# Kernel optimization log

Hardware: AMD Instinct MI355X
Metric: run time of the kernel (lower is better)

Reference implementation:

```python
import jax, jax.numpy as jnp
import numpy as np


def _segsum(x):
    """Stable segment-sum. x: (..., l) -> (..., l, l) lower-triangular sums."""
    l = x.shape[-1]
    cs = jnp.cumsum(x, axis=-1)
    seg = cs[..., :, None] - cs[..., None, :]
    mask = jnp.tril(jnp.ones((l, l), dtype=bool))
    return jnp.where(mask, seg, -jnp.inf)


def setup_inputs() -> dict:
    key = jax.random.key(0)
    kx, ka, kb, kc = jax.random.split(key, 4)
    b, s, h, p, n = 4, 8192, 32, 64, 16
    X = jax.random.normal(kx, (b, s, h, p), dtype=jnp.float32)
    # negative A for realistic decaying SSM dynamics / numerical safety
    A = -jnp.abs(jax.random.normal(ka, (b, s, h), dtype=jnp.float32)) * 0.5
    B = jax.random.normal(kb, (b, s, h, n), dtype=jnp.float32)
    C = jax.random.normal(kc, (b, s, h, n), dtype=jnp.float32)
    return {"X": X, "A": A, "B": B, "C": C, "block_len": 64}


def reference(X, A, B, C, block_len):
    b, s, h, p = X.shape
    n = B.shape[-1]
    c = s // block_len
    l = block_len
    # chunk: (b, c, l, ...)
    Xb = X.reshape(b, c, l, h, p)
    Bb = B.reshape(b, c, l, h, n)
    Cb = C.reshape(b, c, l, h, n)
    Ab = A.reshape(b, c, l, h).transpose(0, 3, 1, 2)  # (b, h, c, l)
    A_cumsum = jnp.cumsum(Ab, axis=-1)                # (b, h, c, l)

    # 1) intra-chunk (diagonal) output
    L = jnp.exp(_segsum(Ab))                          # (b, h, c, l, l)
    Y_diag = jnp.einsum("bclhn,bcshn,bhcls,bcshp->bclhp", Cb, Bb, L, Xb)

    # 2) intra-chunk states (chunk-final state contribution)
    decay_states = jnp.exp(A_cumsum[..., -1:] - A_cumsum)   # (b, h, c, l)
    states = jnp.einsum("bclhn,bhcl,bclhp->bchpn", Bb, decay_states, Xb)

    # 3) inter-chunk recurrence (zero initial states)
    A_last = A_cumsum[..., -1]                        # (b, h, c)
    decay_chunk = jnp.exp(_segsum(jnp.pad(A_last, ((0, 0), (0, 0), (1, 0)))))  # (b,h,c+1,c+1)
    states = jnp.concatenate([jnp.zeros_like(states[:, :1]), states], axis=1)  # (b,c+1,h,p,n)
    new_states = jnp.einsum("bhzc,bchpn->bzhpn", decay_chunk, states)
    states = new_states[:, :-1]                       # states entering each chunk

    # 4) state -> output (off-diagonal)
    state_decay_out = jnp.exp(A_cumsum)               # (b, h, c, l)
    Y_off = jnp.einsum("bclhn,bchpn,bhcl->bclhp", Cb, states, state_decay_out)

    Y = (Y_diag + Y_off).reshape(b, s, h, p)
    return Y
```

## Files before the change

kernel.cpp:

```cpp
#include <hip/hip_runtime.h>

#define BB 4
#define SS 8192
#define HH 32
#define PP 64
#define NN 16
#define LL 64
#define CC 128
#define NCHAIN (BB * HH)
#define NCHT (NCHAIN * CC)

typedef __attribute__((ext_vector_type(8))) short bf16x8;
typedef __attribute__((ext_vector_type(4))) short bf16x4;
typedef __attribute__((ext_vector_type(4))) float f32x4;

__device__ inline short f2bf(float f) {
    unsigned u = __builtin_bit_cast(unsigned, f);
    u = (u + 0x7FFFu + ((u >> 16) & 1u)) >> 16;
    return (short)u;
}

__global__ __launch_bounds__(256) void k1_states(
    const float* __restrict__ X, const float* __restrict__ A,
    const float* __restrict__ B, float* __restrict__ states,
    float* __restrict__ alast_g)
{
    int blk = blockIdx.x;
    int h = blk & (HH - 1);
    int c = (blk >> 5) & (CC - 1);
    int b = blk >> 12;
    int tid = threadIdx.x;
    int w = tid >> 6, l = tid & 63, g = l >> 4, lr = l & 15;
    int chain = b * HH + h;

    __shared__ float Bs[LL][17];

    size_t row0 = (size_t)b * SS + (size_t)c * LL;
    const float* Xp = X + (row0 * HH + h) * PP;
    const float* Bp = B + (row0 * HH + h) * NN;
    const float* Ap = A + row0 * HH + h;

    float av = Ap[(size_t)l * HH];
    int r = tid >> 2, q = tid & 3;
    float4 br = *(const float4*)(Bp + (size_t)r * (HH * NN) + q * 4);
    float xr[16];
#pragma unroll
    for (int kt = 0; kt < 2; ++kt)
#pragma unroll
        for (int e = 0; e < 8; ++e)
            xr[kt * 8 + e] = Xp[(size_t)(kt * 32 + g * 8 + e) * (HH * PP) + 16 * w + lr];

    float x = av;
#pragma unroll
    for (int d = 1; d < 64; d <<= 1) {
        float t = __shfl_up(x, d, 64);
        if (l >= d) x += t;
    }
    float alast = __shfl(x, 63, 64);

    float wlr = __expf(alast - __shfl(x, r & 63, 64));
    Bs[r][q * 4 + 0] = br.x * wlr;
    Bs[r][q * 4 + 1] = br.y * wlr;
    Bs[r][q * 4 + 2] = br.z * wlr;
    Bs[r][q * 4 + 3] = br.w * wlr;
    __syncthreads();

    bf16x8 bt[2], xf[2];
#pragma unroll
    for (int kt = 0; kt < 2; ++kt)
#pragma unroll
        for (int e = 0; e < 8; ++e) {
            int row = kt * 32 + g * 8 + e;
            bt[kt][e] = f2bf(Bs[row][lr]);
            xf[kt][e] = f2bf(xr[kt * 8 + e]);
        }
    f32x4 st = __builtin_amdgcn_mfma_f32_16x16x32_bf16(bt[0], xf[0], (f32x4)0.f, 0, 0, 0);
    st = __builtin_amdgcn_mfma_f32_16x16x32_bf16(bt[1], xf[1], st, 0, 0, 0);

    float4 pv = {st[0], st[1], st[2], st[3]};
    *(float4*)(states + (size_t)(chain * CC + c) * (PP * NN) + (16 * w + lr) * NN + 4 * g) = pv;
    if (tid == 0) alast_g[chain * CC + c] = alast;
}

__global__ __launch_bounds__(256) void k2_scan(
    float* __restrict__ states, const float* __restrict__ alast_g)
{
    int chain = blockIdx.x >> 2;
    int t = ((blockIdx.x & 3) << 8) + threadIdx.x;
    __shared__ float eal[CC];
    if (threadIdx.x < CC)
        eal[threadIdx.x] = __expf(alast_g[chain * CC + threadIdx.x]);
    __syncthreads();

    float* base = states + (size_t)chain * CC * (PP * NN) + t;
    float P = 0.f;
    for (int c0 = 0; c0 < CC; c0 += 8) {
        float s[8], o[8];
#pragma unroll
        for (int u = 0; u < 8; ++u) s[u] = base[(size_t)(c0 + u) * (PP * NN)];
#pragma unroll
        for (int u = 0; u < 8; ++u) { o[u] = P; P = eal[c0 + u] * P + s[u]; }
#pragma unroll
        for (int u = 0; u < 8; ++u) base[(size_t)(c0 + u) * (PP * NN)] = o[u];
    }
}

__global__ __launch_bounds__(256) void k3_y(
    const float* __restrict__ X, const float* __restrict__ A,
    const float* __restrict__ Bm, const float* __restrict__ Cm,
    const float* __restrict__ pin, float* __restrict__ Y)
{
    int blk = blockIdx.x;
    int h = blk & (HH - 1);
    int c = (blk >> 5) & (CC - 1);
    int b = blk >> 12;
    int tid = threadIdx.x;
    int w = tid >> 6, l = tid & 63, g = l >> 4, lr = l & 15;
    int chain = b * HH + h;

    __shared__ short XTF[8 * 64 * 8];
    __shared__ short ScF[8 * 64 * 8];
    __shared__ short BsF[4 * 64 * 8];
    __shared__ short PF[4 * 64 * 8];

    size_t row0 = (size_t)b * SS + (size_t)c * LL;
    const float* Xp = X + (row0 * HH + h) * PP;
    const float* Bp = Bm + (row0 * HH + h) * NN;
    const float* Cp = Cm + (row0 * HH + h) * NN;
    const float* Ap = A + row0 * HH + h;
    float* Yp = Y + (row0 * HH + h) * PP;

    float av = Ap[(size_t)l * HH];
    int r = tid >> 2, q = tid & 3;
    float4 br = *(const float4*)(Bp + (size_t)r * (HH * NN) + q * 4);
    float4 cr0 = {0,0,0,0}, cr1 = {0,0,0,0};
    if (g < 2) {
        const float* crp = Cp + (size_t)(16 * w + lr) * (HH * NN) + g * 8;
        cr0 = *(const float4*)crp;
        cr1 = *(const float4*)(crp + 4);
    }
    float4 pinv = *(const float4*)(pin + (size_t)(chain * CC + c) * (PP * NN) + (16 * w + lr) * NN + 4 * g);
    float xr[16];
#pragma unroll
    for (int si = 0; si < 2; ++si) {
        int k0 = si * 32 + g * 8;
#pragma unroll
        for (int e = 0; e < 8; ++e)
            xr[si * 8 + e] = Xp[(size_t)(k0 + e) * (HH * PP) + 16 * w + lr];
    }

    float x = av;
#pragma unroll
    for (int d = 1; d < 64; d <<= 1) {
        float t = __shfl_up(x, d, 64);
        if (l >= d) x += t;
    }
    float cs_i[4], ei[4];
    int ib = 16 * w + 4 * g;
#pragma unroll
    for (int rr = 0; rr < 4; ++rr) {
        cs_i[rr] = __shfl(x, ib + rr, 64);
        ei[rr] = __expf(cs_i[rr]);
    }

    ((bf16x8*)ScF)[tid] = (bf16x8)0;
    ((bf16x8*)ScF)[tid + 256] = (bf16x8)0;
    if (tid < 128)
        ((bf16x8*)PF)[(tid >> 5) * 64 + 32 + (tid & 31)] = (bf16x8)0;
    {
        int fl = (r & 15) + 16 * (q >> 1);
        int jt = r >> 4;
        bf16x4 bb = { f2bf(br.x), f2bf(br.y), f2bf(br.z), f2bf(br.w) };
        ((bf16x4*)BsF)[(jt * 64 + fl) * 2 + (q & 1)] = bb;
        int zt = tid >> 6, zu = (tid >> 1) & 31, zv = tid & 1;
        ((bf16x4*)BsF)[(zt * 64 + 32 + zu) * 2 + zv] = (bf16x4)0;
    }
    {
        float P4[4] = {pinv.x, pinv.y, pinv.z, pinv.w};
#pragma unroll
        for (int rr = 0; rr < 4; ++rr) {
            int n = 4 * g + rr;
            PF[(w * 64 + (n >> 3) * 16 + lr) * 8 + (n & 7)] = f2bf(P4[rr]);
        }
    }
    bf16x8 caw = (bf16x8)0;
    if (g < 2) {
        caw[0] = f2bf(cr0.x); caw[1] = f2bf(cr0.y);
        caw[2] = f2bf(cr0.z); caw[3] = f2bf(cr0.w);
        caw[4] = f2bf(cr1.x); caw[5] = f2bf(cr1.y);
        caw[6] = f2bf(cr1.z); caw[7] = f2bf(cr1.w);
    }
    __syncthreads();

    f32x4 acc[4];
#pragma unroll
    for (int pt = 0; pt < 4; ++pt) {
        bf16x8 pfv = ((bf16x8*)PF)[pt * 64 + l];
        acc[pt] = __builtin_amdgcn_mfma_f32_16x16x32_bf16(caw, pfv, (f32x4)0.f, 0, 0, 0);
    }
#pragma unroll
    for (int pt = 0; pt < 4; ++pt)
#pragma unroll
        for (int rr = 0; rr < 4; ++rr) acc[pt][rr] *= ei[rr];

    for (int jt = 0; jt <= w; ++jt) {
        bf16x8 bw = ((bf16x8*)BsF)[jt * 64 + l];
        f32x4 sr = __builtin_amdgcn_mfma_f32_16x16x32_bf16(caw, bw, (f32x4)0.f, 0, 0, 0);
        int j = jt * 16 + lr;
        float csj = __shfl(x, j, 64);
        int kt2 = j >> 5;
        int flb = 16 * ((j >> 3) & 3);
#pragma unroll
        for (int rr = 0; rr < 4; ++rr) {
            int i15 = g * 4 + rr;
            int i = 16 * w + i15;
            float v = (j <= i) ? sr[rr] * __expf(cs_i[rr] - csj) : 0.f;
            ScF[((w * 2 + kt2) * 64 + i15 + flb) * 8 + (j & 7)] = f2bf(v);
        }
    }

#pragma unroll
    for (int si = 0; si < 2; ++si) {
        bf16x8 xb;
#pragma unroll
        for (int e = 0; e < 8; ++e) xb[e] = f2bf(xr[si * 8 + e]);
        ((bf16x8*)XTF)[tid + si * 256] = xb;
    }
    __syncthreads();

    int kts = (w >= 2) ? 2 : 1;
    for (int kt = 0; kt < kts; ++kt) {
        bf16x8 af = ((bf16x8*)ScF)[(w * 2 + kt) * 64 + l];
#pragma unroll
        for (int pt = 0; pt < 4; ++pt) {
            bf16x8 xf = ((bf16x8*)XTF)[(kt * 4 + pt) * 64 + l];
            acc[pt] = __builtin_amdgcn_mfma_f32_16x16x32_bf16(af, xf, acc[pt], 0, 0, 0);
        }
    }

#pragma unroll
    for (int pt = 0; pt < 4; ++pt)
#pragma unroll
        for (int rr = 0; rr < 4; ++rr)
            Yp[(size_t)(16 * w + 4 * g + rr) * (HH * PP) + pt * 16 + lr] = acc[pt][rr];
}

extern "C" void kernel_launch(void* const* d_in, const int* in_sizes, int n_in,
                              void* d_out, int out_size, void* d_ws, size_t ws_size,
                              hipStream_t stream)
{
    const float* X = (const float*)d_in[0];
    const float* A = (const float*)d_in[1];
    const float* B = (const float*)d_in[2];
    const float* C = (const float*)d_in[3];
    float* Y = (float*)d_out;

    float* states = (float*)d_ws;
    float* alast  = states + (size_t)NCHT * (PP * NN);

    dim3 blk(256);
    k1_states<<<dim3(NCHT), blk, 0, stream>>>(X, A, B, states, alast);
    k2_scan<<<dim3(NCHAIN * 4), blk, 0, stream>>>(states, alast);
    k3_y<<<dim3(NCHT), blk, 0, stream>>>(X, A, B, C, states, Y);
}
```

Before: 276.3 us.

## Process two chunks per block in state and output kernels to raise loads in flight

k1_states and k3_y now each handle two chunks per block, chunk cp and chunk cp+64 of the same chain, so their grids are halved. All global loads for both chunks (X, A, B, C and incoming states) are issued up front into registers, and the shared-memory staging is reused sequentially for the two chunks. The aim is more memory-level parallelism and less per-block setup in these bandwidth-bound kernels. In exchange, register pressure roughly doubles and the block count falls, which can lower occupancy.

```diff
diff --git a/kernel.cpp b/kernel.cpp
--- a/kernel.cpp
+++ b/kernel.cpp
@@ -20,6 +20,16 @@
     return (short)u;
 }
 
+__device__ inline float wscan(float v, int l) {
+    float x = v;
+#pragma unroll
+    for (int d = 1; d < 64; d <<= 1) {
+        float t = __shfl_up(x, d, 64);
+        if (l >= d) x += t;
+    }
+    return x;
+}
+
 __global__ __launch_bounds__(256) void k1_states(
     const float* __restrict__ X, const float* __restrict__ A,
     const float* __restrict__ B, float* __restrict__ states,
@@ -27,59 +37,69 @@
 {
     int blk = blockIdx.x;
     int h = blk & (HH - 1);
-    int c = (blk >> 5) & (CC - 1);
-    int b = blk >> 12;
+    int cp = (blk >> 5) & 63;
+    int b = blk >> 11;
     int tid = threadIdx.x;
     int w = tid >> 6, l = tid & 63, g = l >> 4, lr = l & 15;
     int chain = b * HH + h;
-
-    __shared__ float Bs[LL][17];
-
-    size_t row0 = (size_t)b * SS + (size_t)c * LL;
-    const float* Xp = X + (row0 * HH + h) * PP;
-    const float* Bp = B + (row0 * HH + h) * NN;
-    const float* Ap = A + row0 * HH + h;
-
-    float av = Ap[(size_t)l * HH];
     int r = tid >> 2, q = tid & 3;
-    float4 br = *(const float4*)(Bp + (size_t)r * (HH * NN) + q * 4);
-    float xr[16];
-#pragma unroll
-    for (int kt = 0; kt < 2; ++kt)
-#pragma unroll
-        for (int e = 0; e < 8; ++e)
-            xr[kt * 8 + e] = Xp[(size_t)(kt * 32 + g * 8 + e) * (HH * PP) + 16 * w + lr];
-
-    float x = av;
-#pragma unroll
-    for (int d = 1; d < 64; d <<= 1) {
-        float t = __shfl_up(x, d, 64);
-        if (l >= d) x += t;
-    }
-    float alast = __shfl(x, 63, 64);
-
-    float wlr = __expf(alast - __shfl(x, r & 63, 64));
-    Bs[r][q * 4 + 0] = br.x * wlr;
-    Bs[r][q * 4 + 1] = br.y * wlr;
-    Bs[r][q * 4 + 2] = br.z * wlr;
-    Bs[r][q * 4 + 3] = br.w * wlr;
-    __syncthreads();
-
-    bf16x8 bt[2], xf[2];
-#pragma unroll
-    for (int kt = 0; kt < 2; ++kt)
-#pragma unroll
-        for (int e = 0; e < 8; ++e) {
-            int row = kt * 32 + g * 8 + e;
-            bt[kt][e] = f2bf(Bs[row][lr]);
-            xf[kt][e] = f2bf(xr[kt * 8 + e]);
-        }
-    f32x4 st = __builtin_amdgcn_mfma_f32_16x16x32_bf16(bt[0], xf[0], (f32x4)0.f, 0, 0, 0);
-    st = __builtin_amdgcn_mfma_f32_16x16x32_bf16(bt[1], xf[1], st, 0, 0, 0);
-
-    float4 pv = {st[0], st[1], st[2], st[3]};
-    *(float4*)(states + (size_t)(chain * CC + c) * (PP * NN) + (16 * w + lr) * NN + 4 * g) = pv;
-    if (tid == 0) alast_g[chain * CC + c] = alast;
+
+    __shared__ float Bs[2][LL][17];
+
+    size_t r0 = (size_t)b * SS + (size_t)cp * LL;
+    size_t r1 = r0 + (size_t)64 * LL;
+    const float* Xp0 = X + (r0 * HH + h) * PP;
+    const float* Xp1 = X + (r1 * HH + h) * PP;
+
+    float av0 = (A + r0 * HH + h)[(size_t)l * HH];
+    float av1 = (A + r1 * HH + h)[(size_t)l * HH];
+    float4 br0 = *(const float4*)(B + (r0 * HH + h) * NN + (size_t)r * (HH * NN) + q * 4);
+    float4 br1 = *(const float4*)(B + (r1 * HH + h) * NN + (size_t)r * (HH * NN) + q * 4);
+    float xr0[16], xr1[16];
+#pragma unroll
+    for (int kt = 0; kt < 2; ++kt)
+#pragma unroll
+        for (int e = 0; e < 8; ++e)
+            xr0[kt * 8 + e] = Xp0[(size_t)(kt * 32 + g * 8 + e) * (HH * PP) + 16 * w + lr];
+#pragma unroll
+    for (int kt = 0; kt < 2; ++kt)
+#pragma unroll
+        for (int e = 0; e < 8; ++e)
+            xr1[kt * 8 + e] = Xp1[(size_t)(kt * 32 + g * 8 + e) * (HH * PP) + 16 * w + lr];
+
+    float x0 = wscan(av0, l), x1 = wscan(av1, l);
+    float alast0 = __shfl(x0, 63, 64), alast1 = __shfl(x1, 63, 64);
+    float w0 = __expf(alast0 - __shfl(x0, r, 64));
+    float w1 = __expf(alast1 - __shfl(x1, r, 64));
+    Bs[0][r][q * 4 + 0] = br0.x * w0;
+    Bs[0][r][q * 4 + 1] = br0.y * w0;
+    Bs[0][r][q * 4 + 2] = br0.z * w0;
+    Bs[0][r][q * 4 + 3] = br0.w * w0;
+    Bs[1][r][q * 4 + 0] = br1.x * w1;
+    Bs[1][r][q * 4 + 1] = br1.y * w1;
+    Bs[1][r][q * 4 + 2] = br1.z * w1;
+    Bs[1][r][q * 4 + 3] = br1.w * w1;
+    __syncthreads();
+
+#define K1_CHUNK(U, xr_, c_) { \
+    bf16x8 bt0, bt1, xf0, xf1; \
+    _Pragma("unroll") for (int e = 0; e < 8; ++e) { \
+        bt0[e] = f2bf(Bs[U][g * 8 + e][lr]); \
+        bt1[e] = f2bf(Bs[U][32 + g * 8 + e][lr]); \
+        xf0[e] = f2bf(xr_[e]); xf1[e] = f2bf(xr_[8 + e]); } \
+    f32x4 st = __builtin_amdgcn_mfma_f32_16x16x32_bf16(bt0, xf0, (f32x4)0.f, 0, 0, 0); \
+    st = __builtin_amdgcn_mfma_f32_16x16x32_bf16(bt1, xf1, st, 0, 0, 0); \
+    float4 pv = {st[0], st[1], st[2], st[3]}; \
+    *(float4*)(states + (size_t)(chain * CC + (c_)) * (PP * NN) + (16 * w + lr) * NN + 4 * g) = pv; }
+
+    K1_CHUNK(0, xr0, cp)
+    K1_CHUNK(1, xr1, cp + 64)
+#undef K1_CHUNK
+
+    if (tid == 0) {
+        alast_g[chain * CC + cp] = alast0;
+        alast_g[chain * CC + cp + 64] = alast1;
+    }
 }
 
 __global__ __launch_bounds__(256) void k2_scan(
@@ -112,137 +132,140 @@
 {
     int blk = blockIdx.x;
     int h = blk & (HH - 1);
-    int c = (blk >> 5) & (CC - 1);
-    int b = blk >> 12;
+    int cp = (blk >> 5) & 63;
+    int b = blk >> 11;
     int tid = threadIdx.x;
     int w = tid >> 6, l = tid & 63, g = l >> 4, lr = l & 15;
     int chain = b * HH + h;
+    int r = tid >> 2, q = tid & 3;
 
     __shared__ short XTF[8 * 64 * 8];
     __shared__ short ScF[8 * 64 * 8];
     __shared__ short BsF[4 * 64 * 8];
     __shared__ short PF[4 * 64 * 8];
 
-    size_t row0 = (size_t)b * SS + (size_t)c * LL;
-    const float* Xp = X + (row0 * HH + h) * PP;
-    const float* Bp = Bm + (row0 * HH + h) * NN;
-    const float* Cp = Cm + (row0 * HH + h) * NN;
-    const float* Ap = A + row0 * HH + h;
-    float* Yp = Y + (row0 * HH + h) * PP;
-
-    float av = Ap[(size_t)l * HH];
-    int r = tid >> 2, q = tid & 3;
-    float4 br = *(const float4*)(Bp + (size_t)r * (HH * NN) + q * 4);
-    float4 cr0 = {0,0,0,0}, cr1 = {0,0,0,0};
+    size_t r0 = (size_t)b * SS + (size_t)cp * LL;
+    size_t r1 = r0 + (size_t)64 * LL;
+    const float* Xp0 = X + (r0 * HH + h) * PP;
+    const float* Xp1 = X + (r1 * HH + h) * PP;
+    float* Yp0 = Y + (r0 * HH + h) * PP;
+    float* Yp1 = Y + (r1 * HH + h) * PP;
+
+    float av0 = (A + r0 * HH + h)[(size_t)l * HH];
+    float av1 = (A + r1 * HH + h)[(size_t)l * HH];
+    float4 br0 = *(const float4*)(Bm + (r0 * HH + h) * NN + (size_t)r * (HH * NN) + q * 4);
+    float4 br1 = *(const float4*)(Bm + (r1 * HH + h) * NN + (size_t)r * (HH * NN) + q * 4);
+    float4 cr00 = {0,0,0,0}, cr10 = {0,0,0,0}, cr01 = {0,0,0,0}, cr11 = {0,0,0,0};
     if (g < 2) {
-        const float* crp = Cp + (size_t)(16 * w + lr) * (HH * NN) + g * 8;
-        cr0 = *(const float4*)crp;
-        cr1 = *(const float4*)(crp + 4);
-    }
-    float4 pinv = *(const float4*)(pin + (size_t)(chain * CC + c) * (PP * NN) + (16 * w + lr) * NN + 4 * g);
-    float xr[16];
-#pragma unroll
-    for (int si = 0; si < 2; ++si) {
-        int k0 = si * 32 + g * 8;
-#pragma unroll
-        for (int e = 0; e < 8; ++e)
-            xr[si * 8 + e] = Xp[(size_t)(k0 + e) * (HH * PP) + 16 * w + lr];
-    }
-
-    float x = av;
-#pragma unroll
-    for (int d = 1; d < 64; d <<= 1) {
-        float t = __shfl_up(x, d, 64);
-        if (l >= d) x += t;
-    }
-    float cs_i[4], ei[4];
-    int ib = 16 * w + 4 * g;
-#pragma unroll
-    for (int rr = 0; rr < 4; ++rr) {
-        cs_i[rr] = __shfl(x, ib + rr, 64);
-        ei[rr] = __expf(cs_i[rr]);
-    }
-
-    ((bf16x8*)ScF)[tid] = (bf16x8)0;
-    ((bf16x8*)ScF)[tid + 256] = (bf16x8)0;
+        const float* cp0 = Cm + (r0 * HH + h) * NN + (size_t)(16 * w + lr) * (HH * NN) + g * 8;
+        const float* cp1 = Cm + (r1 * HH + h) * NN + (size_t)(16 * w + lr) * (HH * NN) + g * 8;
+        cr00 = *(const float4*)cp0; cr10 = *(const float4*)(cp0 + 4);
+        cr01 = *(const float4*)cp1; cr11 = *(const float4*)(cp1 + 4);
+    }
+    int pnoff = (16 * w + lr) * NN + 4 * g;
+    float4 pinv0 = *(const float4*)(pin + (size_t)(chain * CC + cp) * (PP * NN) + pnoff);
+    float4 pinv1 = *(const float4*)(pin + (size_t)(chain * CC + cp + 64) * (PP * NN) + pnoff);
+    float xr0[16], xr1[16];
+#pragma unroll
+    for (int kt = 0; kt < 2; ++kt)
+#pragma unroll
+        for (int e = 0; e < 8; ++e)
+            xr0[kt * 8 + e] = Xp0[(size_t)(kt * 32 + g * 8 + e) * (HH * PP) + 16 * w + lr];
+#pragma unroll
+    for (int kt = 0; kt < 2; ++kt)
+#pragma unroll
+        for (int e = 0; e < 8; ++e)
+            xr1[kt * 8 + e] = Xp1[(size_t)(kt * 32 + g * 8 + e) * (HH * PP) + 16 * w + lr];
+
+    float x0 = wscan(av0, l), x1 = wscan(av1, l);
+
+    ((bf16x8*)ScF)[w * 128 + l] = (bf16x8)0;
+    ((bf16x8*)ScF)[w * 128 + 64 + l] = (bf16x8)0;
     if (tid < 128)
         ((bf16x8*)PF)[(tid >> 5) * 64 + 32 + (tid & 31)] = (bf16x8)0;
     {
-        int fl = (r & 15) + 16 * (q >> 1);
-        int jt = r >> 4;
-        bf16x4 bb = { f2bf(br.x), f2bf(br.y), f2bf(br.z), f2bf(br.w) };
-        ((bf16x4*)BsF)[(jt * 64 + fl) * 2 + (q & 1)] = bb;
         int zt = tid >> 6, zu = (tid >> 1) & 31, zv = tid & 1;
         ((bf16x4*)BsF)[(zt * 64 + 32 + zu) * 2 + zv] = (bf16x4)0;
     }
-    {
-        float P4[4] = {pinv.x, pinv.y, pinv.z, pinv.w};
-#pragma unroll
-        for (int rr = 0; rr < 4; ++rr) {
-            int n = 4 * g + rr;
-            PF[(w * 64 + (n >> 3) * 16 + lr) * 8 + (n & 7)] = f2bf(P4[rr]);
-        }
-    }
-    bf16x8 caw = (bf16x8)0;
-    if (g < 2) {
-        caw[0] = f2bf(cr0.x); caw[1] = f2bf(cr0.y);
-        caw[2] = f2bf(cr0.z); caw[3] = f2bf(cr0.w);
-        caw[4] = f2bf(cr1.x); caw[5] = f2bf(cr1.y);
-        caw[6] = f2bf(cr1.z); caw[7] = f2bf(cr1.w);
-    }
-    __syncthreads();
-
+
+    bf16x8 caw;
     f32x4 acc[4];
-#pragma unroll
-    for (int pt = 0; pt < 4; ++pt) {
-        bf16x8 pfv = ((bf16x8*)PF)[pt * 64 + l];
-        acc[pt] = __builtin_amdgcn_mfma_f32_16x16x32_bf16(caw, pfv, (f32x4)0.f, 0, 0, 0);
-    }
-#pragma unroll
-    for (int pt = 0; pt < 4; ++pt)
-#pragma unroll
-        for (int rr = 0; rr < 4; ++rr) acc[pt][rr] *= ei[rr];
-
-    for (int jt = 0; jt <= w; ++jt) {
-        bf16x8 bw = ((bf16x8*)BsF)[jt * 64 + l];
-        f32x4 sr = __builtin_amdgcn_mfma_f32_16x16x32_bf16(caw, bw, (f32x4)0.f, 0, 0, 0);
-        int j = jt * 16 + lr;
-        float csj = __shfl(x, j, 64);
-        int kt2 = j >> 5;
-        int flb = 16 * ((j >> 3) & 3);
-#pragma unroll
-        for (int rr = 0; rr < 4; ++rr) {
-            int i15 = g * 4 + rr;
-            int i = 16 * w + i15;
-            float v = (j <= i) ? sr[rr] * __expf(cs_i[rr] - csj) : 0.f;
-            ScF[((w * 2 + kt2) * 64 + i15 + flb) * 8 + (j & 7)] = f2bf(v);
-        }
-    }
-
-#pragma unroll
-    for (int si = 0; si < 2; ++si) {
-        bf16x8 xb;
-#pragma unroll
-        for (int e = 0; e < 8; ++e) xb[e] = f2bf(xr[si * 8 + e]);
-        ((bf16x8*)XTF)[tid + si * 256] = xb;
-    }
-    __syncthreads();
-
-    int kts = (w >= 2) ? 2 : 1;
-    for (int kt = 0; kt < kts; ++kt) {
-        bf16x8 af = ((bf16x8*)ScF)[(w * 2 + kt) * 64 + l];
-#pragma unroll
-        for (int pt = 0; pt < 4; ++pt) {
-            bf16x8 xf = ((bf16x8*)XTF)[(kt * 4 + pt) * 64 + l];
-            acc[pt] = __builtin_amdgcn_mfma_f32_16x16x32_bf16(af, xf, acc[pt], 0, 0, 0);
-        }
-    }
-
-#pragma unroll
-    for (int pt = 0; pt < 4; ++pt)
-#pragma unroll
-        for (int rr = 0; rr < 4; ++rr)
-            Yp[(size_t)(16 * w + 4 * g + rr) * (HH * PP) + pt * 16 + lr] = acc[pt][rr];
+    float cs_i[4], ei[4];
+
+#define K3_STAGE(br_, cr0_, cr1_, pinv_) { \
+    int fl = (r & 15) + 16 * (q >> 1); \
+    int jt = r >> 4; \
+    bf16x4 bb = { f2bf(br_.x), f2bf(br_.y), f2bf(br_.z), f2bf(br_.w) }; \
+    ((bf16x4*)BsF)[(jt * 64 + fl) * 2 + (q & 1)] = bb; \
+    bf16x4 pp = { f2bf(pinv_.x), f2bf(pinv_.y), f2bf(pinv_.z), f2bf(pinv_.w) }; \
+    ((bf16x4*)PF)[(w * 64 + (g >> 1) * 16 + lr) * 2 + (g & 1)] = pp; \
+    caw = (bf16x8)0; \
+    if (g < 2) { \
+        caw[0] = f2bf(cr0_.x); caw[1] = f2bf(cr0_.y); caw[2] = f2bf(cr0_.z); caw[3] = f2bf(cr0_.w); \
+        caw[4] = f2bf(cr1_.x); caw[5] = f2bf(cr1_.y); caw[6] = f2bf(cr1_.z); caw[7] = f2bf(cr1_.w); } }
+
+#define K3_PHASE_A(xs_) { \
+    int ib = 16 * w + 4 * g; \
+    _Pragma("unroll") for (int rr = 0; rr < 4; ++rr) { \
+        cs_i[rr] = __shfl(xs_, ib + rr, 64); ei[rr] = __expf(cs_i[rr]); } \
+    _Pragma("unroll") for (int pt = 0; pt < 4; ++pt) { \
+        bf16x8 pfv = ((bf16x8*)PF)[pt * 64 + l]; \
+        acc[pt] = __builtin_amdgcn_mfma_f32_16x16x32_bf16(caw, pfv, (f32x4)0.f, 0, 0, 0); } \
+    _Pragma("unroll") for (int pt = 0; pt < 4; ++pt) \
+        _Pragma("unroll") for (int rr = 0; rr < 4; ++rr) acc[pt][rr] *= ei[rr]; \
+    for (int jt = 0; jt <= w; ++jt) { \
+        bf16x8 bw = ((bf16x8*)BsF)[jt * 64 + l]; \
+        f32x4 sr = __builtin_amdgcn_mfma_f32_16x16x32_bf16(caw, bw, (f32x4)0.f, 0, 0, 0); \
+        int j = jt * 16 + lr; \
+        float csj = __shfl(xs_, j, 64); \
+        int kt2 = j >> 5; \
+        int flb = 16 * ((j >> 3) & 3); \
+        _Pragma("unroll") for (int rr = 0; rr < 4; ++rr) { \
+            int i15 = g * 4 + rr; \
+            int i = 16 * w + i15; \
+            float v = (j <= i) ? sr[rr] * __expf(cs_i[rr] - csj) : 0.f; \
+            ScF[((w * 2 + kt2) * 64 + i15 + flb) * 8 + (j & 7)] = f2bf(v); } } }
+
+#define K3_CONVERT(xr_) { \
+    bf16x8 xb0, xb1; \
+    _Pragma("unroll") for (int e = 0; e < 8; ++e) { xb0[e] = f2bf(xr_[e]); xb1[e] = f2bf(xr_[8 + e]); } \
+    ((bf16x8*)XTF)[tid] = xb0; \
+    ((bf16x8*)XTF)[tid + 256] = xb1; }
+
+#define K3_PHASE_B() { \
+    int kts = (w >= 2) ? 2 : 1; \
+    for (int kt = 0; kt < kts; ++kt) { \
+        bf16x8 af = ((bf16x8*)ScF)[(w * 2 + kt) * 64 + l]; \
+        _Pragma("unroll") for (int pt = 0; pt < 4; ++pt) { \
+            bf16x8 xf = ((bf16x8*)XTF)[(kt * 4 + pt) * 64 + l]; \
+            acc[pt] = __builtin_amdgcn_mfma_f32_16x16x32_bf16(af, xf, acc[pt], 0, 0, 0); } } }
+
+#define K3_STORE(Yp_) { \
+    _Pragma("unroll") for (int pt = 0; pt < 4; ++pt) \
+        _Pragma("unroll") for (int rr = 0; rr < 4; ++rr) \
+            Yp_[(size_t)(16 * w + 4 * g + rr) * (HH * PP) + pt * 16 + lr] = acc[pt][rr]; }
+
+    K3_STAGE(br0, cr00, cr10, pinv0);
+    __syncthreads();
+    K3_PHASE_A(x0);
+    K3_CONVERT(xr0);
+    __syncthreads();
+    K3_PHASE_B();
+    K3_STORE(Yp0);
+
+    K3_STAGE(br1, cr01, cr11, pinv1);
+    __syncthreads();
+    K3_PHASE_A(x1);
+    K3_CONVERT(xr1);
+    __syncthreads();
+    K3_PHASE_B();
+    K3_STORE(Yp1);
+
+#undef K3_STAGE
+#undef K3_PHASE_A
+#undef K3_CONVERT
+#undef K3_PHASE_B
+#undef K3_STORE
 }
 
 extern "C" void kernel_launch(void* const* d_in, const int* in_sizes, int n_in,
@@ -259,7 +282,7 @@
     float* alast  = states + (size_t)NCHT * (PP * NN);
 
     dim3 blk(256);
-    k1_states<<<dim3(NCHT), blk, 0, stream>>>(X, A, B, states, alast);
+    k1_states<<<dim3(NCHT / 2), blk, 0, stream>>>(X, A, B, states, alast);
     k2_scan<<<dim3(NCHAIN * 4), blk, 0, stream>>>(states, alast);
-    k3_y<<<dim3(NCHT), blk, 0, stream>>>(X, A, B, C, states, Y);
-}
+    k3_y<<<dim3(NCHT / 2), blk, 0, stream>>>(X, A, B, C, states, Y);
+}
```

New measurement: 285.9 us. 1.03x slower.

## Store chunk states in bf16 and cache bf16 X fragments for output kernel

Applied to the files above, without the earlier changes.

Chunk states are now written and scanned in bf16 instead of fp32, halving the states traffic in k1, k2 and k3. When the workspace is large enough, k1 also writes the bf16 X fragments in MFMA layout, so k3 reads them contiguously instead of re-reading strided fp32 X. This adds a fresh 128 MB write in k1 and a 128 MB read in k3, in place of k3's 256 MB strided fp32 read. The scan now rounds to bf16 at every step, which may cost accuracy.

```diff
diff --git a/kernel.cpp b/kernel.cpp
--- a/kernel.cpp
+++ b/kernel.cpp
@@ -11,7 +11,7 @@
 #define NCHT (NCHAIN * CC)
 
 typedef __attribute__((ext_vector_type(8))) short bf16x8;
-typedef __attribute__((ext_vector_type(4))) short bf16x4;
+typedef __attribute__((ext_vector_type(4))) short s16x4;
 typedef __attribute__((ext_vector_type(4))) float f32x4;
 
 __device__ inline short f2bf(float f) {
@@ -19,11 +19,24 @@
     u = (u + 0x7FFFu + ((u >> 16) & 1u)) >> 16;
     return (short)u;
 }
+__device__ inline float bf2f(short s) {
+    unsigned u = ((unsigned)(unsigned short)s) << 16;
+    return __builtin_bit_cast(float, u);
+}
+__device__ inline float wscan(float v, int l) {
+    float x = v;
+#pragma unroll
+    for (int d = 1; d < 64; d <<= 1) {
+        float t = __shfl_up(x, d, 64);
+        if (l >= d) x += t;
+    }
+    return x;
+}
 
 __global__ __launch_bounds__(256) void k1_states(
     const float* __restrict__ X, const float* __restrict__ A,
-    const float* __restrict__ B, float* __restrict__ states,
-    float* __restrict__ alast_g)
+    const float* __restrict__ B, short* __restrict__ states,
+    float* __restrict__ alast_g, short* __restrict__ xtf, int do_xtf)
 {
     int blk = blockIdx.x;
     int h = blk & (HH - 1);
@@ -32,6 +45,7 @@
     int tid = threadIdx.x;
     int w = tid >> 6, l = tid & 63, g = l >> 4, lr = l & 15;
     int chain = b * HH + h;
+    int r = tid >> 2, q = tid & 3;
 
     __shared__ float Bs[LL][17];
 
@@ -41,7 +55,6 @@
     const float* Ap = A + row0 * HH + h;
 
     float av = Ap[(size_t)l * HH];
-    int r = tid >> 2, q = tid & 3;
     float4 br = *(const float4*)(Bp + (size_t)r * (HH * NN) + q * 4);
     float xr[16];
 #pragma unroll
@@ -50,40 +63,39 @@
         for (int e = 0; e < 8; ++e)
             xr[kt * 8 + e] = Xp[(size_t)(kt * 32 + g * 8 + e) * (HH * PP) + 16 * w + lr];
 
-    float x = av;
-#pragma unroll
-    for (int d = 1; d < 64; d <<= 1) {
-        float t = __shfl_up(x, d, 64);
-        if (l >= d) x += t;
-    }
+    float x = wscan(av, l);
     float alast = __shfl(x, 63, 64);
-
-    float wlr = __expf(alast - __shfl(x, r & 63, 64));
+    float wlr = __expf(alast - __shfl(x, r, 64));
     Bs[r][q * 4 + 0] = br.x * wlr;
     Bs[r][q * 4 + 1] = br.y * wlr;
     Bs[r][q * 4 + 2] = br.z * wlr;
     Bs[r][q * 4 + 3] = br.w * wlr;
     __syncthreads();
 
-    bf16x8 bt[2], xf[2];
-#pragma unroll
-    for (int kt = 0; kt < 2; ++kt)
-#pragma unroll
-        for (int e = 0; e < 8; ++e) {
-            int row = kt * 32 + g * 8 + e;
-            bt[kt][e] = f2bf(Bs[row][lr]);
-            xf[kt][e] = f2bf(xr[kt * 8 + e]);
-        }
-    f32x4 st = __builtin_amdgcn_mfma_f32_16x16x32_bf16(bt[0], xf[0], (f32x4)0.f, 0, 0, 0);
-    st = __builtin_amdgcn_mfma_f32_16x16x32_bf16(bt[1], xf[1], st, 0, 0, 0);
-
-    float4 pv = {st[0], st[1], st[2], st[3]};
-    *(float4*)(states + (size_t)(chain * CC + c) * (PP * NN) + (16 * w + lr) * NN + 4 * g) = pv;
+    bf16x8 bt0, bt1, xf0, xf1;
+#pragma unroll
+    for (int e = 0; e < 8; ++e) {
+        bt0[e] = f2bf(Bs[g * 8 + e][lr]);
+        bt1[e] = f2bf(Bs[32 + g * 8 + e][lr]);
+        xf0[e] = f2bf(xr[e]);
+        xf1[e] = f2bf(xr[8 + e]);
+    }
+    f32x4 st = __builtin_amdgcn_mfma_f32_16x16x32_bf16(bt0, xf0, (f32x4)0.f, 0, 0, 0);
+    st = __builtin_amdgcn_mfma_f32_16x16x32_bf16(bt1, xf1, st, 0, 0, 0);
+
+    s16x4 sp = { f2bf(st[0]), f2bf(st[1]), f2bf(st[2]), f2bf(st[3]) };
+    *(s16x4*)(states + (((size_t)(chain * CC + c)) << 10) + ((16 * w + lr) << 4) + (g << 2)) = sp;
+
+    if (do_xtf) {
+        short* xd = xtf + (((size_t)(chain * CC + c)) << 12);
+        ((bf16x8*)xd)[tid] = xf0;
+        ((bf16x8*)xd)[tid + 256] = xf1;
+    }
     if (tid == 0) alast_g[chain * CC + c] = alast;
 }
 
 __global__ __launch_bounds__(256) void k2_scan(
-    float* __restrict__ states, const float* __restrict__ alast_g)
+    short* __restrict__ states, const float* __restrict__ alast_g)
 {
     int chain = blockIdx.x >> 2;
     int t = ((blockIdx.x & 3) << 8) + threadIdx.x;
@@ -92,23 +104,25 @@
         eal[threadIdx.x] = __expf(alast_g[chain * CC + threadIdx.x]);
     __syncthreads();
 
-    float* base = states + (size_t)chain * CC * (PP * NN) + t;
+    short* base = states + ((size_t)chain * CC << 10) + t;
     float P = 0.f;
     for (int c0 = 0; c0 < CC; c0 += 8) {
-        float s[8], o[8];
-#pragma unroll
-        for (int u = 0; u < 8; ++u) s[u] = base[(size_t)(c0 + u) * (PP * NN)];
-#pragma unroll
-        for (int u = 0; u < 8; ++u) { o[u] = P; P = eal[c0 + u] * P + s[u]; }
-#pragma unroll
-        for (int u = 0; u < 8; ++u) base[(size_t)(c0 + u) * (PP * NN)] = o[u];
-    }
-}
-
-__global__ __launch_bounds__(256) void k3_y(
-    const float* __restrict__ X, const float* __restrict__ A,
-    const float* __restrict__ Bm, const float* __restrict__ Cm,
-    const float* __restrict__ pin, float* __restrict__ Y)
+        short s[8];
+#pragma unroll
+        for (int u = 0; u < 8; ++u) s[u] = base[(size_t)(c0 + u) << 10];
+#pragma unroll
+        for (int u = 0; u < 8; ++u) {
+            float o = P;
+            P = eal[c0 + u] * P + bf2f(s[u]);
+            base[(size_t)(c0 + u) << 10] = f2bf(o);
+        }
+    }
+}
+
+__global__ __launch_bounds__(256) void k3_big(
+    const float* __restrict__ A, const float* __restrict__ Bm,
+    const float* __restrict__ Cm, const short* __restrict__ pin,
+    const short* __restrict__ xtf, float* __restrict__ Y)
 {
     int blk = blockIdx.x;
     int h = blk & (HH - 1);
@@ -117,6 +131,7 @@
     int tid = threadIdx.x;
     int w = tid >> 6, l = tid & 63, g = l >> 4, lr = l & 15;
     int chain = b * HH + h;
+    int r = tid >> 2, q = tid & 3;
 
     __shared__ short XTF[8 * 64 * 8];
     __shared__ short ScF[8 * 64 * 8];
@@ -124,14 +139,15 @@
     __shared__ short PF[4 * 64 * 8];
 
     size_t row0 = (size_t)b * SS + (size_t)c * LL;
-    const float* Xp = X + (row0 * HH + h) * PP;
     const float* Bp = Bm + (row0 * HH + h) * NN;
     const float* Cp = Cm + (row0 * HH + h) * NN;
     const float* Ap = A + row0 * HH + h;
     float* Yp = Y + (row0 * HH + h) * PP;
-
+    const short* xsrc = xtf + (((size_t)(chain * CC + c)) << 12);
+
+    bf16x8 xv0 = ((const bf16x8*)xsrc)[tid];
+    bf16x8 xv1 = ((const bf16x8*)xsrc)[tid + 256];
     float av = Ap[(size_t)l * HH];
-    int r = tid >> 2, q = tid & 3;
     float4 br = *(const float4*)(Bp + (size_t)r * (HH * NN) + q * 4);
     float4 cr0 = {0,0,0,0}, cr1 = {0,0,0,0};
     if (g < 2) {
@@ -139,50 +155,28 @@
         cr0 = *(const float4*)crp;
         cr1 = *(const float4*)(crp + 4);
     }
-    float4 pinv = *(const float4*)(pin + (size_t)(chain * CC + c) * (PP * NN) + (16 * w + lr) * NN + 4 * g);
-    float xr[16];
-#pragma unroll
-    for (int si = 0; si < 2; ++si) {
-        int k0 = si * 32 + g * 8;
-#pragma unroll
-        for (int e = 0; e < 8; ++e)
-            xr[si * 8 + e] = Xp[(size_t)(k0 + e) * (HH * PP) + 16 * w + lr];
-    }
-
-    float x = av;
-#pragma unroll
-    for (int d = 1; d < 64; d <<= 1) {
-        float t = __shfl_up(x, d, 64);
-        if (l >= d) x += t;
-    }
-    float cs_i[4], ei[4];
-    int ib = 16 * w + 4 * g;
-#pragma unroll
-    for (int rr = 0; rr < 4; ++rr) {
-        cs_i[rr] = __shfl(x, ib + rr, 64);
-        ei[rr] = __expf(cs_i[rr]);
-    }
-
-    ((bf16x8*)ScF)[tid] = (bf16x8)0;
-    ((bf16x8*)ScF)[tid + 256] = (bf16x8)0;
+    s16x4 pinb = *(const s16x4*)(pin + (((size_t)(chain * CC + c)) << 10) + ((16 * w + lr) << 4) + (g << 2));
+
+    float x = wscan(av, l);
+
+    ((bf16x8*)ScF)[w * 128 + l] = (bf16x8)0;
+    ((bf16x8*)ScF)[w * 128 + 64 + l] = (bf16x8)0;
     if (tid < 128)
         ((bf16x8*)PF)[(tid >> 5) * 64 + 32 + (tid & 31)] = (bf16x8)0;
     {
+        int zt = tid >> 6, zu = (tid >> 1) & 31, zv = tid & 1;
+        ((s16x4*)BsF)[(zt * 64 + 32 + zu) * 2 + zv] = (s16x4)0;
+    }
+
+    ((bf16x8*)XTF)[tid] = xv0;
+    ((bf16x8*)XTF)[tid + 256] = xv1;
+    {
         int fl = (r & 15) + 16 * (q >> 1);
         int jt = r >> 4;
-        bf16x4 bb = { f2bf(br.x), f2bf(br.y), f2bf(br.z), f2bf(br.w) };
-        ((bf16x4*)BsF)[(jt * 64 + fl) * 2 + (q & 1)] = bb;
-        int zt = tid >> 6, zu = (tid >> 1) & 31, zv = tid & 1;
-        ((bf16x4*)BsF)[(zt * 64 + 32 + zu) * 2 + zv] = (bf16x4)0;
-    }
-    {
-        float P4[4] = {pinv.x, pinv.y, pinv.z, pinv.w};
-#pragma unroll
-        for (int rr = 0; rr < 4; ++rr) {
-            int n = 4 * g + rr;
-            PF[(w * 64 + (n >> 3) * 16 + lr) * 8 + (n & 7)] = f2bf(P4[rr]);
-        }
-    }
+        s16x4 bb = { f2bf(br.x), f2bf(br.y), f2bf(br.z), f2bf(br.w) };
+        ((s16x4*)BsF)[(jt * 64 + fl) * 2 + (q & 1)] = bb;
+    }
+    *(s16x4*)&PF[(w * 64 + (g >> 1) * 16 + lr) * 8 + (g & 1) * 4] = pinb;
     bf16x8 caw = (bf16x8)0;
     if (g < 2) {
         caw[0] = f2bf(cr0.x); caw[1] = f2bf(cr0.y);
@@ -191,6 +185,14 @@
         caw[6] = f2bf(cr1.z); caw[7] = f2bf(cr1.w);
     }
     __syncthreads();
+
+    float cs_i[4], ei[4];
+    int ib = 16 * w + 4 * g;
+#pragma unroll
+    for (int rr = 0; rr < 4; ++rr) {
+        cs_i[rr] = __shfl(x, ib + rr, 64);
+        ei[rr] = __expf(cs_i[rr]);
+    }
 
     f32x4 acc[4];
 #pragma unroll
@@ -219,6 +221,126 @@
         }
     }
 
+    int kts = (w >= 2) ? 2 : 1;
+    for (int kt = 0; kt < kts; ++kt) {
+        bf16x8 af = ((bf16x8*)ScF)[(w * 2 + kt) * 64 + l];
+#pragma unroll
+        for (int pt = 0; pt < 4; ++pt) {
+            bf16x8 xf = ((bf16x8*)XTF)[(kt * 4 + pt) * 64 + l];
+            acc[pt] = __builtin_amdgcn_mfma_f32_16x16x32_bf16(af, xf, acc[pt], 0, 0, 0);
+        }
+    }
+
+#pragma unroll
+    for (int pt = 0; pt < 4; ++pt)
+#pragma unroll
+        for (int rr = 0; rr < 4; ++rr)
+            Yp[(size_t)(16 * w + 4 * g + rr) * (HH * PP) + pt * 16 + lr] = acc[pt][rr];
+}
+
+__global__ __launch_bounds__(256) void k3_small(
+    const float* __restrict__ X, const float* __restrict__ A,
+    const float* __restrict__ Bm, const float* __restrict__ Cm,
+    const short* __restrict__ pin, float* __restrict__ Y)
+{
+    int blk = blockIdx.x;
+    int h = blk & (HH - 1);
+    int c = (blk >> 5) & (CC - 1);
+    int b = blk >> 12;
+    int tid = threadIdx.x;
+    int w = tid >> 6, l = tid & 63, g = l >> 4, lr = l & 15;
+    int chain = b * HH + h;
+    int r = tid >> 2, q = tid & 3;
+
+    __shared__ short XTF[8 * 64 * 8];
+    __shared__ short ScF[8 * 64 * 8];
+    __shared__ short BsF[4 * 64 * 8];
+    __shared__ short PF[4 * 64 * 8];
+
+    size_t row0 = (size_t)b * SS + (size_t)c * LL;
+    const float* Xp = X + (row0 * HH + h) * PP;
+    const float* Bp = Bm + (row0 * HH + h) * NN;
+    const float* Cp = Cm + (row0 * HH + h) * NN;
+    const float* Ap = A + row0 * HH + h;
+    float* Yp = Y + (row0 * HH + h) * PP;
+
+    float av = Ap[(size_t)l * HH];
+    float4 br = *(const float4*)(Bp + (size_t)r * (HH * NN) + q * 4);
+    float4 cr0 = {0,0,0,0}, cr1 = {0,0,0,0};
+    if (g < 2) {
+        const float* crp = Cp + (size_t)(16 * w + lr) * (HH * NN) + g * 8;
+        cr0 = *(const float4*)crp;
+        cr1 = *(const float4*)(crp + 4);
+    }
+    s16x4 pinb = *(const s16x4*)(pin + (((size_t)(chain * CC + c)) << 10) + ((16 * w + lr) << 4) + (g << 2));
+    float xr[16];
+#pragma unroll
+    for (int si = 0; si < 2; ++si)
+#pragma unroll
+        for (int e = 0; e < 8; ++e)
+            xr[si * 8 + e] = Xp[(size_t)(si * 32 + g * 8 + e) * (HH * PP) + 16 * w + lr];
+
+    float x = wscan(av, l);
+
+    ((bf16x8*)ScF)[w * 128 + l] = (bf16x8)0;
+    ((bf16x8*)ScF)[w * 128 + 64 + l] = (bf16x8)0;
+    if (tid < 128)
+        ((bf16x8*)PF)[(tid >> 5) * 64 + 32 + (tid & 31)] = (bf16x8)0;
+    {
+        int zt = tid >> 6, zu = (tid >> 1) & 31, zv = tid & 1;
+        ((s16x4*)BsF)[(zt * 64 + 32 + zu) * 2 + zv] = (s16x4)0;
+    }
+    {
+        int fl = (r & 15) + 16 * (q >> 1);
+        int jt = r >> 4;
+        s16x4 bb = { f2bf(br.x), f2bf(br.y), f2bf(br.z), f2bf(br.w) };
+        ((s16x4*)BsF)[(jt * 64 + fl) * 2 + (q & 1)] = bb;
+    }
+    *(s16x4*)&PF[(w * 64 + (g >> 1) * 16 + lr) * 8 + (g & 1) * 4] = pinb;
+    bf16x8 caw = (bf16x8)0;
+    if (g < 2) {
+        caw[0] = f2bf(cr0.x); caw[1] = f2bf(cr0.y);
+        caw[2] = f2bf(cr0.z); caw[3] = f2bf(cr0.w);
+        caw[4] = f2bf(cr1.x); caw[5] = f2bf(cr1.y);
+        caw[6] = f2bf(cr1.z); caw[7] = f2bf(cr1.w);
+    }
+    __syncthreads();
+
+    float cs_i[4], ei[4];
+    int ib = 16 * w + 4 * g;
+#pragma unroll
+    for (int rr = 0; rr < 4; ++rr) {
+        cs_i[rr] = __shfl(x, ib + rr, 64);
+        ei[rr] = __expf(cs_i[rr]);
+    }
+
+    f32x4 acc[4];
+#pragma unroll
+    for (int pt = 0; pt < 4; ++pt) {
+        bf16x8 pfv = ((bf16x8*)PF)[pt * 64 + l];
+        acc[pt] = __builtin_amdgcn_mfma_f32_16x16x32_bf16(caw, pfv, (f32x4)0.f, 0, 0, 0);
+    }
+#pragma unroll
+    for (int pt = 0; pt < 4; ++pt)
+#pragma unroll
+        for (int rr = 0; rr < 4; ++rr) acc[pt][rr] *= ei[rr];
+
+    for (int jt = 0; jt <= w; ++jt) {
+        bf16x8 bw = ((bf16x8*)BsF)[jt * 64 + l];
+        f32x4 sr = __builtin_amdgcn_mfma_f32_16x16x32_bf16(caw, bw, (f32x4)0.f, 0, 0, 0);
+        int j = jt * 16 + lr;
+        float csj = __shfl(x, j, 64);
+        int kt2 = j >> 5;
+        int flb = 16 * ((j >> 3) & 3);
+#pragma unroll
+        for (int rr = 0; rr < 4; ++rr) {
+            int i15 = g * 4 + rr;
+            int i = 16 * w + i15;
+            float v = (j <= i) ? sr[rr] * __expf(cs_i[rr] - csj) : 0.f;
+            ScF[((w * 2 + kt2) * 64 + i15 + flb) * 8 + (j & 7)] = f2bf(v);
+        }
+    }
+
 #pragma unroll
     for (int si = 0; si < 2; ++si) {
         bf16x8 xb;
@@ -255,11 +377,19 @@
     const float* C = (const float*)d_in[3];
     float* Y = (float*)d_out;
 
-    float* states = (float*)d_ws;
-    float* alast  = states + (size_t)NCHT * (PP * NN);
+    const size_t states_bytes = (size_t)NCHT * 1024 * 2;
+    const size_t alast_bytes  = (size_t)NCHT * 4;
+    const size_t xtf_bytes    = (size_t)NCHT * 4096 * 2;
+    short* states = (short*)d_ws;
+    float* alast  = (float*)((char*)d_ws + states_bytes);
+    short* xtf    = (short*)((char*)d_ws + states_bytes + alast_bytes);
+    int big = (ws_size >= states_bytes + alast_bytes + xtf_bytes) ? 1 : 0;
 
     dim3 blk(256);
-    k1_states<<<dim3(NCHT), blk, 0, stream>>>(X, A, B, states, alast);
+    k1_states<<<dim3(NCHT), blk, 0, stream>>>(X, A, B, states, alast, xtf, big);
     k2_scan<<<dim3(NCHAIN * 4), blk, 0, stream>>>(states, alast);
-    k3_y<<<dim3(NCHT), blk, 0, stream>>>(X, A, B, C, states, Y);
-}
+    if (big)
+        k3_big<<<dim3(NCHT), blk, 0, stream>>>(A, B, C, states, xtf, Y);
+    else
+        k3_small<<<dim3(NCHT), blk, 0, stream>>>(X, A, B, C, states, Y);
+}
```

After: 267.2 us. -3.3%, faster.
